# Kernel tuning notes

Hardware: AMD Instinct MI355X
Metric: run time of the kernel (lower is better)

Reference implementation:

```python
import jax, jax.numpy as jnp
import numpy as np

N_NODES = 50000
N_FEAT = 256
N_HID = 32
N_HEADS = 8
N_CLASSES = 32
N_EDGES = 800000
NEG_SLOPE = 0.2  # PyG GATConv default leaky_relu slope


def setup_inputs() -> dict:
    key = jax.random.key(0)
    ks = jax.random.split(key, 10)
    x = jax.random.normal(ks[0], (N_NODES, N_FEAT), dtype=jnp.float32)
    edge_index = jax.random.randint(ks[1], (2, N_EDGES), 0, N_NODES, dtype=jnp.int64)
    s1 = 1.0 / np.sqrt(N_FEAT)
    s2 = 1.0 / np.sqrt(N_HID * N_HEADS)
    W1 = jax.random.normal(ks[2], (N_FEAT, N_HEADS * N_HID), dtype=jnp.float32) * s1
    a_src1 = jax.random.normal(ks[3], (N_HEADS, N_HID), dtype=jnp.float32) * s1
    a_dst1 = jax.random.normal(ks[4], (N_HEADS, N_HID), dtype=jnp.float32) * s1
    b1 = jnp.zeros((N_HEADS * N_HID,), dtype=jnp.float32)
    W2 = jax.random.normal(ks[5], (N_HEADS * N_HID, N_CLASSES), dtype=jnp.float32) * s2
    a_src2 = jax.random.normal(ks[6], (1, N_CLASSES), dtype=jnp.float32) * s2
    a_dst2 = jax.random.normal(ks[7], (1, N_CLASSES), dtype=jnp.float32) * s2
    b2 = jnp.zeros((N_CLASSES,), dtype=jnp.float32)
    return {"x": x, "edge_index": edge_index, "W1": W1, "a_src1": a_src1,
            "a_dst1": a_dst1, "b1": b1, "W2": W2, "a_src2": a_src2,
            "a_dst2": a_dst2, "b2": b2}


def _gat_conv(h, src, dst, n_nodes, W, a_src, a_dst, heads, ch):
    # h: [N, F_in]; returns [N, heads, ch] aggregated per-node features
    z = (h @ W).reshape(n_nodes, heads, ch)           # [N,H,C]
    alpha_src = jnp.einsum('nhc,hc->nh', z, a_src)    # [N,H]
    alpha_dst = jnp.einsum('nhc,hc->nh', z, a_dst)    # [N,H]
    logits = jax.nn.leaky_relu(alpha_src[src] + alpha_dst[dst], NEG_SLOPE)  # [E,H]
    # segment softmax over incoming edges of each dst node
    m = jax.ops.segment_max(logits, dst, num_segments=n_nodes)  # [N,H]
    e = jnp.exp(logits - m[dst])                                 # [E,H]
    denom = jax.ops.segment_sum(e, dst, num_segments=n_nodes)   # [N,H]
    alpha = e / denom[dst]                                       # [E,H]
    msg = z[src] * alpha[:, :, None]                             # [E,H,C]
    return jax.ops.segment_sum(msg, dst, num_segments=n_nodes)  # [N,H,C]


def reference(x, edge_index, W1, a_src1, a_dst1, b1, W2, a_src2, a_dst2, b2):
    n = x.shape[0]
    # PyG GATConv default: add self loops
    loops = jnp.arange(n, dtype=edge_index.dtype)
    src = jnp.concatenate([edge_index[0], loops])
    dst = jnp.concatenate([edge_index[1], loops])
    h1 = _gat_conv(x, src, dst, n, W1, a_src1, a_dst1, N_HEADS, N_HID)
    h1 = h1.reshape(n, N_HEADS * N_HID) + b1          # concat=True
    h1 = jax.nn.elu(h1)
    # dropout is a no-op in eval mode
    h2 = _gat_conv(h1, src, dst, n, W2, a_src2, a_dst2, 1, N_CLASSES)
    out = h2.mean(axis=1) + b2                        # concat=False, heads=1
    return out
```

## Files before the change

kernel.cpp:

```cpp
#include <hip/hip_runtime.h>

#define NNODES 50000
#define NFEAT 256
#define NHID 32
#define NHEADS 8
#define NCLASSES 32
#define NEDGES 800000
#define ETOT (NEDGES + NNODES)
#define NSCAN_BLK 196
#define GEMM1_BLKS 782
#define SCAT_BLKS 3321

typedef __attribute__((ext_vector_type(8))) short short8;
typedef __attribute__((ext_vector_type(4))) float f32x4;

__device__ __forceinline__ void get_edge(const int* __restrict__ ei, int e,
                                         int& s, int& d) {
    if (e < NEDGES) { s = ei[e]; d = ei[NEDGES + e]; }
    else            { s = e - NEDGES; d = s; }
}
__device__ __forceinline__ float lrelu(float x) { return x > 0.f ? x : 0.2f * x; }
__device__ __forceinline__ unsigned short f2bf(float f) {
    unsigned u = __float_as_uint(f);
    unsigned r = u + 0x7fffu + ((u >> 16) & 1u);
    return (unsigned short)(r >> 16);
}
__device__ __forceinline__ float bflo(unsigned u) { return __uint_as_float(u << 16); }
__device__ __forceinline__ float bfhi(unsigned u) { return __uint_as_float(u & 0xffff0000u); }

__global__ void wprep_hist_k(const float* __restrict__ W1, const float* __restrict__ W2,
                             short8* __restrict__ W1frag, short8* __restrict__ W2frag,
                             const int* __restrict__ ei, int* __restrict__ deg) {
    if (blockIdx.x < 36) {
        int idx = blockIdx.x * 256 + threadIdx.x;
        if (idx < 8192) {
            int kc = idx >> 10, r = idx & 1023;
            int nt = r >> 6, lane = r & 63;
            int l16 = lane & 15, quad = lane >> 4;
            int n = nt * 16 + l16, k0 = kc * 32 + quad * 8;
            short8 v;
#pragma unroll
            for (int j = 0; j < 8; ++j) v[j] = (short)f2bf(W1[(k0 + j) * 256 + n]);
            W1frag[idx] = v;
        } else if (idx < 8192 + 1024) {
            int g = idx - 8192;
            int kc = g >> 7, r = g & 127;
            int nt = r >> 6, lane = r & 63;
            int l16 = lane & 15, quad = lane >> 4;
            int n = nt * 16 + l16, k0 = kc * 32 + quad * 8;
            short8 v;
#pragma unroll
            for (int j = 0; j < 8; ++j) v[j] = (short)f2bf(W2[(k0 + j) * 32 + n]);
            W2frag[g] = v;
        }
    } else {
        int e = (blockIdx.x - 36) * 256 + threadIdx.x;
        if (e >= ETOT) return;
        int s, d;
        get_edge(ei, e, s, d);
        atomicAdd(&deg[d], 1);
    }
}

__global__ void scan_part_k(const int* __restrict__ deg, int* __restrict__ row_local,
                            int* __restrict__ bsum) {
    __shared__ int ws[4];
    int t = threadIdx.x, lane = t & 63, wid = t >> 6;
    int idx = blockIdx.x * 256 + t;
    int v = (idx < NNODES) ? deg[idx] : 0;
    int inc = v;
#pragma unroll
    for (int off = 1; off < 64; off <<= 1) {
        int u = __shfl_up(inc, off, 64);
        if (lane >= off) inc += u;
    }
    if (lane == 63) ws[wid] = inc;
    __syncthreads();
    int woff = 0;
#pragma unroll
    for (int j = 0; j < 4; ++j) woff += (j < wid) ? ws[j] : 0;
    if (idx < NNODES) row_local[idx] = woff + inc - v;
    if (t == 255) bsum[blockIdx.x] = woff + inc;
}

__global__ void scan_fix_k(const int* __restrict__ row_local, const int* __restrict__ bsum,
                           int* __restrict__ row_start) {
    __shared__ int ws[4];
    __shared__ int sboff;
    int t = threadIdx.x, lane = t & 63, wid = t >> 6;
    int v = (t < NSCAN_BLK) ? bsum[t] : 0;
    int inc = v;
#pragma unroll
    for (int off = 1; off < 64; off <<= 1) {
        int u = __shfl_up(inc, off, 64);
        if (lane >= off) inc += u;
    }
    if (lane == 63) ws[wid] = inc;
    __syncthreads();
    int woff = 0;
#pragma unroll
    for (int j = 0; j < 4; ++j) woff += (j < wid) ? ws[j] : 0;
    if (t == blockIdx.x) sboff = woff + inc - v;
    __syncthreads();
    int idx = blockIdx.x * 256 + t;
    if (idx < NNODES) row_start[idx] = row_local[idx] + sboff;
    if (idx == 0) row_start[NNODES] = ETOT;
}

__global__ __launch_bounds__(256) void gemm1_scatter_k(
        const float* __restrict__ x, const short8* __restrict__ Wfrag,
        const float* __restrict__ av, const float* __restrict__ bv,
        unsigned short* __restrict__ z1, float* __restrict__ as_, float* __restrict__ ad_,
        const int* __restrict__ ei, const int* __restrict__ row_start,
        int* __restrict__ cursor, int* __restrict__ csr_src) {
    __shared__ short8 wlds[1024];
    if (blockIdx.x >= GEMM1_BLKS) {
        int e = (blockIdx.x - GEMM1_BLKS) * 256 + threadIdx.x;
        if (e >= ETOT) return;
        int s, d;
        get_edge(ei, e, s, d);
        int pos = atomicAdd(&cursor[d], 1);
        csr_src[row_start[d] + pos] = s;
        return;
    }
    int t = threadIdx.x;
    int w = t >> 6, lane = t & 63;
    int quad = lane >> 4, l16 = lane & 15;
    int mA = blockIdx.x * 64 + w * 16 + l16;
    int mAl = min(mA, NNODES - 1);

    f32x4 acc[16];
#pragma unroll
    for (int nt = 0; nt < 16; ++nt) acc[nt] = (f32x4){0.f, 0.f, 0.f, 0.f};

    short8 pf[4];
#pragma unroll
    for (int j = 0; j < 4; ++j) pf[j] = Wfrag[j * 256 + t];

    for (int kc = 0; kc < 8; ++kc) {
        __syncthreads();
#pragma unroll
        for (int j = 0; j < 4; ++j) wlds[j * 256 + t] = pf[j];
        __syncthreads();
        if (kc < 7) {
#pragma unroll
            for (int j = 0; j < 4; ++j) pf[j] = Wfrag[(kc + 1) * 1024 + j * 256 + t];
        }
        int k0 = kc * 32 + quad * 8;
        const float4* xp = (const float4*)(x + (size_t)mAl * 256 + k0);
        float4 a0 = xp[0], a1 = xp[1];
        short8 af;
        af[0] = (short)f2bf(a0.x); af[1] = (short)f2bf(a0.y);
        af[2] = (short)f2bf(a0.z); af[3] = (short)f2bf(a0.w);
        af[4] = (short)f2bf(a1.x); af[5] = (short)f2bf(a1.y);
        af[6] = (short)f2bf(a1.z); af[7] = (short)f2bf(a1.w);
#pragma unroll
        for (int nt = 0; nt < 16; ++nt) {
            short8 bf8 = wlds[nt * 64 + lane];
            acc[nt] = __builtin_amdgcn_mfma_f32_16x16x32_bf16(af, bf8, acc[nt], 0, 0, 0);
        }
    }
    int mrow0 = blockIdx.x * 64 + w * 16 + quad * 4;
#pragma unroll
    for (int nt = 0; nt < 16; ++nt) {
        int n = nt * 16 + l16;
#pragma unroll
        for (int r = 0; r < 4; ++r) {
            int mr = mrow0 + r;
            if (mr < NNODES) z1[(size_t)mr * 256 + n] = f2bf(acc[nt][r]);
        }
    }
#pragma unroll
    for (int h = 0; h < 8; ++h) {
        float av0 = av[(2 * h) * 16 + l16], av1v = av[(2 * h + 1) * 16 + l16];
        float bv0 = bv[(2 * h) * 16 + l16], bv1v = bv[(2 * h + 1) * 16 + l16];
#pragma unroll
        for (int r = 0; r < 4; ++r) {
            float pa = acc[2 * h][r] * av0 + acc[2 * h + 1][r] * av1v;
            float pb = acc[2 * h][r] * bv0 + acc[2 * h + 1][r] * bv1v;
#pragma unroll
            for (int off = 1; off < 16; off <<= 1) {
                pa += __shfl_xor(pa, off, 64);
                pb += __shfl_xor(pb, off, 64);
            }
            int mr = mrow0 + r;
            if (l16 == 0 && mr < NNODES) { as_[mr * 8 + h] = pa; ad_[mr * 8 + h] = pb; }
        }
    }
}

__global__ __launch_bounds__(256) void gemm2_mfma_k(
        const unsigned short* __restrict__ h1, const short8* __restrict__ Wfrag,
        const float* __restrict__ av, const float* __restrict__ bv,
        unsigned short* __restrict__ z2b, float* __restrict__ as_, float* __restrict__ ad_) {
    int w = threadIdx.x >> 6, lane = threadIdx.x & 63;
    int quad = lane >> 4, l16 = lane & 15;
    int mA = blockIdx.x * 64 + w * 16 + l16;
    int mAl = min(mA, NNODES - 1);

    f32x4 acc[2];
    acc[0] = (f32x4){0.f, 0.f, 0.f, 0.f};
    acc[1] = (f32x4){0.f, 0.f, 0.f, 0.f};
    for (int kc = 0; kc < 8; ++kc) {
        int k0 = kc * 32 + quad * 8;
        short8 af = *(const short8*)(h1 + (size_t)mAl * 256 + k0);
#pragma unroll
        for (int nt = 0; nt < 2; ++nt) {
            short8 bf8 = Wfrag[kc * 128 + nt * 64 + lane];
            acc[nt] = __builtin_amdgcn_mfma_f32_16x16x32_bf16(af, bf8, acc[nt], 0, 0, 0);
        }
    }
    int mrow0 = blockIdx.x * 64 + w * 16 + quad * 4;
    float av0 = av[l16], av1v = av[16 + l16];
    float bv0 = bv[l16], bv1v = bv[16 + l16];
#pragma unroll
    for (int r = 0; r < 4; ++r) {
        int mr = mrow0 + r;
        float pa = acc[0][r] * av0 + acc[1][r] * av1v;
        float pb = acc[0][r] * bv0 + acc[1][r] * bv1v;
#pragma unroll
        for (int off = 1; off < 16; off <<= 1) {
            pa += __shfl_xor(pa, off, 64);
            pb += __shfl_xor(pb, off, 64);
        }
        if (mr < NNODES) {
            z2b[(size_t)mr * 32 + l16] = f2bf(acc[0][r]);
            z2b[(size_t)mr * 32 + 16 + l16] = f2bf(acc[1][r]);
            if (l16 == 0) { as_[mr] = pa; ad_[mr] = pb; }
        }
    }
}

__global__ void agg1_csr_k(const int* __restrict__ row_start, const int* __restrict__ csr_src,
                           const unsigned short* __restrict__ z, const float* __restrict__ as_,
                           const float* __restrict__ ad_, const float* __restrict__ b,
                           unsigned short* __restrict__ h1) {
    int wv = threadIdx.x >> 6, lane = threadIdx.x & 63;
    int d = blockIdx.x * 4 + wv;
    int h = lane >> 3;
    int c0 = lane * 4;
    int e8 = lane & 7;
    float adh = ad_[d * 8 + h];
    int beg = row_start[d], end = row_start[d + 1];
    float sum = 0.f, a0 = 0.f, a1 = 0.f, a2 = 0.f, a3 = 0.f;
    int i = beg;
    for (; i + 8 <= end; i += 8) {
        int sv = csr_src[i + e8];
        float myw = __expf(lrelu(as_[sv * 8 + h] + adh));
        int se[8];
        float we[8];
#pragma unroll
        for (int e = 0; e < 8; ++e) {
            se[e] = __shfl(sv, e, 64);
            we[e] = __shfl(myw, (lane & 56) | e, 64);
        }
        uint2 q[8];
#pragma unroll
        for (int e = 0; e < 8; ++e)
            q[e] = *(const uint2*)(z + (size_t)se[e] * 256 + c0);
#pragma unroll
        for (int e = 0; e < 8; ++e) {
            float wgt = we[e];
            sum += wgt;
            a0 += wgt * bflo(q[e].x);
            a1 += wgt * bfhi(q[e].x);
            a2 += wgt * bflo(q[e].y);
            a3 += wgt * bfhi(q[e].y);
        }
    }
    for (; i < end; ++i) {
        int s = csr_src[i];
        float wgt = __expf(lrelu(as_[s * 8 + h] + adh));
        uint2 zz = *(const uint2*)(z + (size_t)s * 256 + c0);
        sum += wgt;
        a0 += wgt * bflo(zz.x);
        a1 += wgt * bfhi(zz.x);
        a2 += wgt * bflo(zz.y);
        a3 += wgt * bfhi(zz.y);
    }
    float inv = 1.f / sum;
    float o0 = a0 * inv + b[c0 + 0];
    float o1 = a1 * inv + b[c0 + 1];
    float o2 = a2 * inv + b[c0 + 2];
    float o3 = a3 * inv + b[c0 + 3];
    o0 = o0 > 0.f ? o0 : expm1f(o0);
    o1 = o1 > 0.f ? o1 : expm1f(o1);
    o2 = o2 > 0.f ? o2 : expm1f(o2);
    o3 = o3 > 0.f ? o3 : expm1f(o3);
    uint2 pk;
    pk.x = (unsigned)f2bf(o0) | ((unsigned)f2bf(o1) << 16);
    pk.y = (unsigned)f2bf(o2) | ((unsigned)f2bf(o3) << 16);
    *(uint2*)(h1 + (size_t)d * 256 + c0) = pk;
}

__global__ void agg2_csr_k(const int* __restrict__ row_start, const int* __restrict__ csr_src,
                           const unsigned short* __restrict__ z2b, const float* __restrict__ as_,
                           const float* __restrict__ ad_, const float* __restrict__ b,
                           float* __restrict__ out) {
    int g = blockIdx.x * 16 + (threadIdx.x >> 4);
    int l = threadIdx.x & 15;
    int lane = threadIdx.x & 63;
    int c0 = l * 2;
    int beg = row_start[g], end = row_start[g + 1];
    float adn = ad_[g];
    int e8 = l & 7;
    int gb = lane & 48;
    float sum = 0.f, a0 = 0.f, a1 = 0.f;
    int i = beg;
    for (; i + 8 <= end; i += 8) {
        int sv = csr_src[i + e8];
        float myw = __expf(lrelu(as_[sv] + adn));
        int se[8];
        float we[8];
#pragma unroll
        for (int e = 0; e < 8; ++e) {
            se[e] = __shfl(sv, gb | e, 64);
            we[e] = __shfl(myw, gb | (8 | e), 64);
        }
        unsigned q[8];
#pragma unroll
        for (int e = 0; e < 8; ++e)
            q[e] = *(const unsigned*)(z2b + (size_t)se[e] * 32 + c0);
#pragma unroll
        for (int e = 0; e < 8; ++e) {
            float wgt = we[e];
            sum += wgt;
            a0 += wgt * bflo(q[e]);
            a1 += wgt * bfhi(q[e]);
        }
    }
    for (; i < end; ++i) {
        int s = csr_src[i];
        float wgt = __expf(lrelu(as_[s] + adn));
        unsigned q = *(const unsigned*)(z2b + (size_t)s * 32 + c0);
        sum += wgt;
        a0 += wgt * bflo(q);
        a1 += wgt * bfhi(q);
    }
    float inv = 1.f / sum;
    float2 o;
    o.x = a0 * inv + b[c0];
    o.y = a1 * inv + b[c0 + 1];
    *(float2*)(out + (size_t)g * 32 + c0) = o;
}

extern "C" void kernel_launch(void* const* d_in, const int* in_sizes, int n_in,
                              void* d_out, int out_size, void* d_ws, size_t ws_size,
                              hipStream_t stream) {
    const float* x   = (const float*)d_in[0];
    const int*   ei  = (const int*)d_in[1];
    const float* W1  = (const float*)d_in[2];
    const float* av1 = (const float*)d_in[3];
    const float* bv1 = (const float*)d_in[4];
    const float* b1  = (const float*)d_in[5];
    const float* W2  = (const float*)d_in[6];
    const float* av2 = (const float*)d_in[7];
    const float* bv2 = (const float*)d_in[8];
    const float* b2  = (const float*)d_in[9];
    float* out = (float*)d_out;

    unsigned short* z1 = (unsigned short*)d_ws;
    unsigned short* h1 = (unsigned short*)((float*)d_ws + 6400000);
    float* as1 = (float*)d_ws + 12800000;
    float* ad1 = as1 + 400000;
    unsigned short* z2b = (unsigned short*)(ad1 + 400000);
    float* as2 = ad1 + 400000 + 800000;
    float* ad2 = as2 + 50000;
    short8* W1frag = (short8*)(ad2 + 50000);
    short8* W2frag = W1frag + 8192;
    int* deg       = (int*)(ad2 + 50000) + 36864;
    int* cursor    = deg + 50000;
    int* row_start = cursor + 50000;
    int* csr_src   = row_start + 50001;
    int* row_local = csr_src + 850000;
    int* bsum      = row_local + 50000;

    hipMemsetAsync(deg, 0, (size_t)100000 * 4, stream);

    wprep_hist_k<<<36 + SCAT_BLKS, 256, 0, stream>>>(W1, W2, W1frag, W2frag, ei, deg);
    scan_part_k<<<NSCAN_BLK, 256, 0, stream>>>(deg, row_local, bsum);
    scan_fix_k<<<NSCAN_BLK, 256, 0, stream>>>(row_local, bsum, row_start);

    gemm1_scatter_k<<<GEMM1_BLKS + SCAT_BLKS, 256, 0, stream>>>(
        x, W1frag, av1, bv1, z1, as1, ad1, ei, row_start, cursor, csr_src);
    agg1_csr_k<<<(NNODES + 3) / 4, 256, 0, stream>>>(row_start, csr_src, z1, as1, ad1, b1, h1);

    gemm2_mfma_k<<<(NNODES + 63) / 64, 256, 0, stream>>>(h1, W2frag, av2, bv2, z2b, as2, ad2);
    agg2_csr_k<<<NNODES / 16, 256, 0, stream>>>(row_start, csr_src, z2b, as2, ad2, b2, out);
}
```

Measured before the change: 294.5 us.

## Store layer-1 features head-major and split aggregation per head; record CSR positions during histogram

After: 362.3 us. +23.0%, slower.

```diff
diff --git a/kernel.cpp b/kernel.cpp
--- a/kernel.cpp
+++ b/kernel.cpp
@@ -10,6 +10,7 @@
 #define NSCAN_BLK 196
 #define GEMM1_BLKS 782
 #define SCAT_BLKS 3321
+#define AGG1_BLKS 100000
 
 typedef __attribute__((ext_vector_type(8))) short short8;
 typedef __attribute__((ext_vector_type(4))) float f32x4;
@@ -30,7 +31,8 @@
 
 __global__ void wprep_hist_k(const float* __restrict__ W1, const float* __restrict__ W2,
                              short8* __restrict__ W1frag, short8* __restrict__ W2frag,
-                             const int* __restrict__ ei, int* __restrict__ deg) {
+                             const int* __restrict__ ei, int* __restrict__ deg,
+                             unsigned short* __restrict__ pos) {
     if (blockIdx.x < 36) {
         int idx = blockIdx.x * 256 + threadIdx.x;
         if (idx < 8192) {
@@ -56,9 +58,8 @@
     } else {
         int e = (blockIdx.x - 36) * 256 + threadIdx.x;
         if (e >= ETOT) return;
-        int s, d;
-        get_edge(ei, e, s, d);
-        atomicAdd(&deg[d], 1);
+        int d = (e < NEDGES) ? ei[NEDGES + e] : (e - NEDGES);
+        pos[e] = (unsigned short)atomicAdd(&deg[d], 1);
     }
 }
 
@@ -110,17 +111,16 @@
 __global__ __launch_bounds__(256) void gemm1_scatter_k(
         const float* __restrict__ x, const short8* __restrict__ Wfrag,
         const float* __restrict__ av, const float* __restrict__ bv,
-        unsigned short* __restrict__ z1, float* __restrict__ as_, float* __restrict__ ad_,
+        unsigned short* __restrict__ z1T, float* __restrict__ asT, float* __restrict__ adT,
         const int* __restrict__ ei, const int* __restrict__ row_start,
-        int* __restrict__ cursor, int* __restrict__ csr_src) {
+        const unsigned short* __restrict__ pos, int* __restrict__ csr_src) {
     __shared__ short8 wlds[1024];
     if (blockIdx.x >= GEMM1_BLKS) {
         int e = (blockIdx.x - GEMM1_BLKS) * 256 + threadIdx.x;
         if (e >= ETOT) return;
         int s, d;
         get_edge(ei, e, s, d);
-        int pos = atomicAdd(&cursor[d], 1);
-        csr_src[row_start[d] + pos] = s;
+        csr_src[row_start[d] + (int)pos[e]] = s;
         return;
     }
     int t = threadIdx.x;
@@ -163,11 +163,12 @@
     int mrow0 = blockIdx.x * 64 + w * 16 + quad * 4;
 #pragma unroll
     for (int nt = 0; nt < 16; ++nt) {
-        int n = nt * 16 + l16;
+        int hh = nt >> 1, cc = (nt & 1) * 16 + l16;
 #pragma unroll
         for (int r = 0; r < 4; ++r) {
             int mr = mrow0 + r;
-            if (mr < NNODES) z1[(size_t)mr * 256 + n] = f2bf(acc[nt][r]);
+            if (mr < NNODES)
+                z1T[((size_t)hh * NNODES + mr) * 32 + cc] = f2bf(acc[nt][r]);
         }
     }
 #pragma unroll
@@ -184,7 +185,10 @@
                 pb += __shfl_xor(pb, off, 64);
             }
             int mr = mrow0 + r;
-            if (l16 == 0 && mr < NNODES) { as_[mr * 8 + h] = pa; ad_[mr * 8 + h] = pb; }
+            if (l16 == 0 && mr < NNODES) {
+                asT[(size_t)h * NNODES + mr] = pa;
+                adT[(size_t)h * NNODES + mr] = pb;
+            }
         }
     }
 }
@@ -231,66 +235,61 @@
     }
 }
 
-__global__ void agg1_csr_k(const int* __restrict__ row_start, const int* __restrict__ csr_src,
-                           const unsigned short* __restrict__ z, const float* __restrict__ as_,
-                           const float* __restrict__ ad_, const float* __restrict__ b,
-                           unsigned short* __restrict__ h1) {
+__global__ __launch_bounds__(256) void agg1_csr_k(
+        const int* __restrict__ row_start, const int* __restrict__ csr_src,
+        const unsigned short* __restrict__ z1T, const float* __restrict__ asT,
+        const float* __restrict__ adT, const float* __restrict__ b,
+        unsigned short* __restrict__ h1) {
+    int h = blockIdx.x & 7;
+    int dblk = blockIdx.x >> 3;
     int wv = threadIdx.x >> 6, lane = threadIdx.x & 63;
-    int d = blockIdx.x * 4 + wv;
-    int h = lane >> 3;
-    int c0 = lane * 4;
-    int e8 = lane & 7;
-    float adh = ad_[d * 8 + h];
+    int d = dblk * 4 + wv;
+    int e8 = lane >> 3, c4 = lane & 7;
+    const float* ash = asT + (size_t)h * NNODES;
+    const unsigned short* zh = z1T + (size_t)h * NNODES * 32;
+    float adh = adT[(size_t)h * NNODES + d];
     int beg = row_start[d], end = row_start[d + 1];
     float sum = 0.f, a0 = 0.f, a1 = 0.f, a2 = 0.f, a3 = 0.f;
-    int i = beg;
-    for (; i + 8 <= end; i += 8) {
-        int sv = csr_src[i + e8];
-        float myw = __expf(lrelu(as_[sv * 8 + h] + adh));
-        int se[8];
-        float we[8];
-#pragma unroll
-        for (int e = 0; e < 8; ++e) {
-            se[e] = __shfl(sv, e, 64);
-            we[e] = __shfl(myw, (lane & 56) | e, 64);
-        }
-        uint2 q[8];
-#pragma unroll
-        for (int e = 0; e < 8; ++e)
-            q[e] = *(const uint2*)(z + (size_t)se[e] * 256 + c0);
-#pragma unroll
-        for (int e = 0; e < 8; ++e) {
-            float wgt = we[e];
-            sum += wgt;
-            a0 += wgt * bflo(q[e].x);
-            a1 += wgt * bfhi(q[e].x);
-            a2 += wgt * bflo(q[e].y);
-            a3 += wgt * bfhi(q[e].y);
-        }
-    }
-    for (; i < end; ++i) {
-        int s = csr_src[i];
-        float wgt = __expf(lrelu(as_[s * 8 + h] + adh));
-        uint2 zz = *(const uint2*)(z + (size_t)s * 256 + c0);
-        sum += wgt;
-        a0 += wgt * bflo(zz.x);
-        a1 += wgt * bfhi(zz.x);
-        a2 += wgt * bflo(zz.y);
-        a3 += wgt * bfhi(zz.y);
-    }
-    float inv = 1.f / sum;
-    float o0 = a0 * inv + b[c0 + 0];
-    float o1 = a1 * inv + b[c0 + 1];
-    float o2 = a2 * inv + b[c0 + 2];
-    float o3 = a3 * inv + b[c0 + 3];
-    o0 = o0 > 0.f ? o0 : expm1f(o0);
-    o1 = o1 > 0.f ? o1 : expm1f(o1);
-    o2 = o2 > 0.f ? o2 : expm1f(o2);
-    o3 = o3 > 0.f ? o3 : expm1f(o3);
-    uint2 pk;
-    pk.x = (unsigned)f2bf(o0) | ((unsigned)f2bf(o1) << 16);
-    pk.y = (unsigned)f2bf(o2) | ((unsigned)f2bf(o3) << 16);
-    *(uint2*)(h1 + (size_t)d * 256 + c0) = pk;
+    for (int i = beg; i < end; i += 16) {
+        int i0 = i + e8, i1 = i + 8 + e8;
+        int s0 = csr_src[i0 < end ? i0 : end - 1];
+        int s1 = csr_src[i1 < end ? i1 : end - 1];
+        float w0 = __expf(lrelu(ash[s0] + adh));
+        float w1 = __expf(lrelu(ash[s1] + adh));
+        w0 = (i0 < end) ? w0 : 0.f;
+        w1 = (i1 < end) ? w1 : 0.f;
+        uint2 q0 = *(const uint2*)(zh + (size_t)s0 * 32 + c4 * 4);
+        uint2 q1 = *(const uint2*)(zh + (size_t)s1 * 32 + c4 * 4);
+        sum += w0 + w1;
+        a0 += w0 * bflo(q0.x) + w1 * bflo(q1.x);
+        a1 += w0 * bfhi(q0.x) + w1 * bfhi(q1.x);
+        a2 += w0 * bflo(q0.y) + w1 * bflo(q1.y);
+        a3 += w0 * bfhi(q0.y) + w1 * bfhi(q1.y);
+    }
+#pragma unroll
+    for (int off = 8; off < 64; off <<= 1) {
+        sum += __shfl_xor(sum, off, 64);
+        a0 += __shfl_xor(a0, off, 64);
+        a1 += __shfl_xor(a1, off, 64);
+        a2 += __shfl_xor(a2, off, 64);
+        a3 += __shfl_xor(a3, off, 64);
+    }
+    if (e8 == 0) {
+        int c0 = h * 32 + c4 * 4;
+        float inv = 1.f / sum;
+        float o0 = a0 * inv + b[c0 + 0];
+        float o1 = a1 * inv + b[c0 + 1];
+        float o2 = a2 * inv + b[c0 + 2];
+        float o3 = a3 * inv + b[c0 + 3];
+        o0 = o0 > 0.f ? o0 : expm1f(o0);
+        o1 = o1 > 0.f ? o1 : expm1f(o1);
+        o2 = o2 > 0.f ? o2 : expm1f(o2);
+        o3 = o3 > 0.f ? o3 : expm1f(o3);
+        uint2 pk;
+        pk.x = (unsigned)f2bf(o0) | ((unsigned)f2bf(o1) << 16);
+        pk.y = (unsigned)f2bf(o2) | ((unsigned)f2bf(o3) << 16);
+        *(uint2*)(h1 + (size_t)d * 256 + c0) = pk;
+    }
 }
 
 __global__ void agg2_csr_k(const int* __restrict__ row_start, const int* __restrict__ csr_src,
@@ -359,7 +358,7 @@
     const float* b2  = (const float*)d_in[9];
     float* out = (float*)d_out;
 
-    unsigned short* z1 = (unsigned short*)d_ws;
+    unsigned short* z1T = (unsigned short*)d_ws;
     unsigned short* h1 = (unsigned short*)((float*)d_ws + 6400000);
     float* as1 = (float*)d_ws + 12800000;
     float* ad1 = as1 + 400000;
@@ -369,21 +368,21 @@
     short8* W1frag = (short8*)(ad2 + 50000);
     short8* W2frag = W1frag + 8192;
     int* deg       = (int*)(ad2 + 50000) + 36864;
-    int* cursor    = deg + 50000;
-    int* row_start = cursor + 50000;
+    int* row_start = deg + 50000;
     int* csr_src   = row_start + 50001;
     int* row_local = csr_src + 850000;
     int* bsum      = row_local + 50000;
-
-    hipMemsetAsync(deg, 0, (size_t)100000 * 4, stream);
-
-    wprep_hist_k<<<36 + SCAT_BLKS, 256, 0, stream>>>(W1, W2, W1frag, W2frag, ei, deg);
+    unsigned short* pos = (unsigned short*)z2b;
+
+    hipMemsetAsync(deg, 0, (size_t)50000 * 4, stream);
+
+    wprep_hist_k<<<36 + SCAT_BLKS, 256, 0, stream>>>(W1, W2, W1frag, W2frag, ei, deg, pos);
     scan_part_k<<<NSCAN_BLK, 256, 0, stream>>>(deg, row_local, bsum);
     scan_fix_k<<<NSCAN_BLK, 256, 0, stream>>>(row_local, bsum, row_start);
 
     gemm1_scatter_k<<<GEMM1_BLKS + SCAT_BLKS, 256, 0, stream>>>(
-        x, W1frag, av1, bv1, z1, as1, ad1, ei, row_start, cursor, csr_src);
-    agg1_csr_k<<<(NNODES + 3) / 4, 256, 0, stream>>>(row_start, csr_src, z1, as1, ad1, b1, h1);
+        x, W1frag, av1, bv1, z1T, as1, ad1, ei, row_start, pos, csr_src);
+    agg1_csr_k<<<AGG1_BLKS, 256, 0, stream>>>(row_start, csr_src, z1T, as1, ad1, b1, h1);
 
     gemm2_mfma_k<<<(NNODES + 63) / 64, 256, 0, stream>>>(h1, W2frag, av2, bv2, z2b, as2, ad2);
     agg2_csr_k<<<NNODES / 16, 256, 0, stream>>>(row_start, csr_src, z2b, as2, ad2, b2, out);
```

## Record edge slots during histogram, drop LDS weight staging, prefetch agg1 edges

Applied to the files above, without the earlier changes.

New measurement: 282.6 us. 1.04x faster.

```diff
diff --git a/kernel.cpp b/kernel.cpp
--- a/kernel.cpp
+++ b/kernel.cpp
@@ -30,7 +30,8 @@
 
 __global__ void wprep_hist_k(const float* __restrict__ W1, const float* __restrict__ W2,
                              short8* __restrict__ W1frag, short8* __restrict__ W2frag,
-                             const int* __restrict__ ei, int* __restrict__ deg) {
+                             const int* __restrict__ ei, int* __restrict__ deg,
+                             unsigned short* __restrict__ pos) {
     if (blockIdx.x < 36) {
         int idx = blockIdx.x * 256 + threadIdx.x;
         if (idx < 8192) {
@@ -56,9 +57,8 @@
     } else {
         int e = (blockIdx.x - 36) * 256 + threadIdx.x;
         if (e >= ETOT) return;
-        int s, d;
-        get_edge(ei, e, s, d);
-        atomicAdd(&deg[d], 1);
+        int d = (e < NEDGES) ? ei[NEDGES + e] : (e - NEDGES);
+        pos[e] = (unsigned short)atomicAdd(&deg[d], 1);
     }
 }
 
@@ -112,15 +112,13 @@
         const float* __restrict__ av, const float* __restrict__ bv,
         unsigned short* __restrict__ z1, float* __restrict__ as_, float* __restrict__ ad_,
         const int* __restrict__ ei, const int* __restrict__ row_start,
-        int* __restrict__ cursor, int* __restrict__ csr_src) {
-    __shared__ short8 wlds[1024];
+        const unsigned short* __restrict__ pos, int* __restrict__ csr_src) {
     if (blockIdx.x >= GEMM1_BLKS) {
         int e = (blockIdx.x - GEMM1_BLKS) * 256 + threadIdx.x;
         if (e >= ETOT) return;
         int s, d;
         get_edge(ei, e, s, d);
-        int pos = atomicAdd(&cursor[d], 1);
-        csr_src[row_start[d] + pos] = s;
+        csr_src[row_start[d] + (int)pos[e]] = s;
         return;
     }
     int t = threadIdx.x;
@@ -129,34 +127,30 @@
     int mA = blockIdx.x * 64 + w * 16 + l16;
     int mAl = min(mA, NNODES - 1);
 
-    f32x4 acc[16];
-#pragma unroll
-    for (int nt = 0; nt < 16; ++nt) acc[nt] = (f32x4){0.f, 0.f, 0.f, 0.f};
-
-    short8 pf[4];
-#pragma unroll
-    for (int j = 0; j < 4; ++j) pf[j] = Wfrag[j * 256 + t];
-
+    const float4* xp = (const float4*)(x + (size_t)mAl * 256);
+    short8 xreg[8];
+#pragma unroll
     for (int kc = 0; kc < 8; ++kc) {
-        __syncthreads();
-#pragma unroll
-        for (int j = 0; j < 4; ++j) wlds[j * 256 + t] = pf[j];
-        __syncthreads();
-        if (kc < 7) {
-#pragma unroll
-            for (int j = 0; j < 4; ++j) pf[j] = Wfrag[(kc + 1) * 1024 + j * 256 + t];
-        }
-        int k0 = kc * 32 + quad * 8;
-        const float4* xp = (const float4*)(x + (size_t)mAl * 256 + k0);
-        float4 a0 = xp[0], a1 = xp[1];
+        float4 a0 = xp[kc * 8 + quad * 2];
+        float4 a1 = xp[kc * 8 + quad * 2 + 1];
         short8 af;
         af[0] = (short)f2bf(a0.x); af[1] = (short)f2bf(a0.y);
         af[2] = (short)f2bf(a0.z); af[3] = (short)f2bf(a0.w);
         af[4] = (short)f2bf(a1.x); af[5] = (short)f2bf(a1.y);
         af[6] = (short)f2bf(a1.z); af[7] = (short)f2bf(a1.w);
+        xreg[kc] = af;
+    }
+
+    f32x4 acc[16];
+#pragma unroll
+    for (int nt = 0; nt < 16; ++nt) acc[nt] = (f32x4){0.f, 0.f, 0.f, 0.f};
+
+#pragma unroll
+    for (int kc = 0; kc < 8; ++kc) {
+        short8 af = xreg[kc];
 #pragma unroll
         for (int nt = 0; nt < 16; ++nt) {
-            short8 bf8 = wlds[nt * 64 + lane];
+            short8 bf8 = Wfrag[kc * 1024 + nt * 64 + lane];
             acc[nt] = __builtin_amdgcn_mfma_f32_16x16x32_bf16(af, bf8, acc[nt], 0, 0, 0);
         }
     }
@@ -243,10 +237,18 @@
     float adh = ad_[d * 8 + h];
     int beg = row_start[d], end = row_start[d + 1];
     float sum = 0.f, a0 = 0.f, a1 = 0.f, a2 = 0.f, a3 = 0.f;
-    int i = beg;
-    for (; i + 8 <= end; i += 8) {
-        int sv = csr_src[i + e8];
-        float myw = __expf(lrelu(as_[sv * 8 + h] + adh));
+
+    int idx = beg + e8;
+    int sv = csr_src[idx < end ? idx : end - 1];
+    float myw = __expf(lrelu(as_[sv * 8 + h] + adh));
+    myw = (idx < end) ? myw : 0.f;
+
+    for (int i = beg; i < end; i += 8) {
+        int idx2 = i + 8 + e8;
+        int sv2 = csr_src[idx2 < end ? idx2 : end - 1];
+        float myw2 = __expf(lrelu(as_[sv2 * 8 + h] + adh));
+        myw2 = (idx2 < end) ? myw2 : 0.f;
+
         int se[8];
         float we[8];
 #pragma unroll
@@ -267,16 +269,8 @@
             a2 += wgt * bflo(q[e].y);
             a3 += wgt * bfhi(q[e].y);
         }
-    }
-    for (; i < end; ++i) {
-        int s = csr_src[i];
-        float wgt = __expf(lrelu(as_[s * 8 + h] + adh));
-        uint2 zz = *(const uint2*)(z + (size_t)s * 256 + c0);
-        sum += wgt;
-        a0 += wgt * bflo(zz.x);
-        a1 += wgt * bfhi(zz.x);
-        a2 += wgt * bflo(zz.y);
-        a3 += wgt * bfhi(zz.y);
+        sv = sv2;
+        myw = myw2;
     }
     float inv = 1.f / sum;
     float o0 = a0 * inv + b[c0 + 0];
@@ -369,20 +363,20 @@
     short8* W1frag = (short8*)(ad2 + 50000);
     short8* W2frag = W1frag + 8192;
     int* deg       = (int*)(ad2 + 50000) + 36864;
-    int* cursor    = deg + 50000;
-    int* row_start = cursor + 50000;
+    int* row_start = deg + 50000;
     int* csr_src   = row_start + 50001;
     int* row_local = csr_src + 850000;
     int* bsum      = row_local + 50000;
-
-    hipMemsetAsync(deg, 0, (size_t)100000 * 4, stream);
-
-    wprep_hist_k<<<36 + SCAT_BLKS, 256, 0, stream>>>(W1, W2, W1frag, W2frag, ei, deg);
+    unsigned short* pos = (unsigned short*)z2b;
+
+    hipMemsetAsync(deg, 0, (size_t)50000 * 4, stream);
+
+    wprep_hist_k<<<36 + SCAT_BLKS, 256, 0, stream>>>(W1, W2, W1frag, W2frag, ei, deg, pos);
     scan_part_k<<<NSCAN_BLK, 256, 0, stream>>>(deg, row_local, bsum);
     scan_fix_k<<<NSCAN_BLK, 256, 0, stream>>>(row_local, bsum, row_start);
 
     gemm1_scatter_k<<<GEMM1_BLKS + SCAT_BLKS, 256, 0, stream>>>(
-        x, W1frag, av1, bv1, z1, as1, ad1, ei, row_start, cursor, csr_src);
+        x, W1frag, av1, bv1, z1, as1, ad1, ei, row_start, pos, csr_src);
     agg1_csr_k<<<(NNODES + 3) / 4, 256, 0, stream>>>(row_start, csr_src, z1, as1, ad1, b1, h1);
 
     gemm2_mfma_k<<<(NNODES + 63) / 64, 256, 0, stream>>>(h1, W2frag, av2, bv2, z2b, as2, ad2);
```
